# Kernel tuning notes

Hardware: AMD Instinct MI355X
Metric: run time of the kernel (lower is better)

## Reference

```python
import jax, jax.numpy as jnp
import numpy as np

N_NODES = 100000
N_EDGES = 1000000
D_FEAT = 64


def setup_inputs() -> dict:
    key = jax.random.key(0)
    k1, k2 = jax.random.split(key)
    x = jax.random.normal(k1, (N_NODES, D_FEAT), dtype=jnp.float32)
    es = jax.random.randint(k2, (2, N_EDGES), 0, N_NODES, dtype=jnp.int32)
    return {"x": x, "es": es}


def reference(x, es):
    # message (option='o2i'): col, row = es ; x_i = x[row], x_o = x[col]
    col, row = es[0], es[1]
    x_i = x[row]                              # [E, D]
    x_o = x[col]                              # [E, D]
    msg = jnp.concatenate([x_i, x_o], axis=-1)  # [E, 2D]
    n = x.shape[0]
    # aggregate: scatter-mean over idx=col
    summed = jax.ops.segment_sum(msg, col, num_segments=n)          # [N, 2D]
    ones = jnp.ones((es.shape[1],), dtype=x.dtype)
    count = jax.ops.segment_sum(ones, col, num_segments=n)          # [N]
    count = jnp.maximum(count, 1.0)[:, None]  # clamp(min=1), broadcast
    return summed / count
```

## Files before the change

### kernel.cpp

```cpp
#include <hip/hip_runtime.h>

#define D 64
#define SH 8
#define CPB 256
#define CH 2048
#define MAXNB 512


__global__ __launch_bounds__(256) void count_kernel(
    const int* __restrict__ es, int* __restrict__ cmat,
    int NB, int NBLK, int E) {
  __shared__ int hist[MAXNB];
  int t = threadIdx.x;
  hist[t] = 0;
  hist[t + 256] = 0;
  __syncthreads();
  int base_e = blockIdx.x * CH;
#pragma unroll
  for (int j = 0; j < 8; j++) {
    int e = base_e + t + j * 256;
    if (e < E) atomicAdd(&hist[es[e] >> SH], 1);
  }
  __syncthreads();
  for (int b = t; b < NB; b += 256) cmat[b * NBLK + blockIdx.x] = hist[b];
}

__global__ __launch_bounds__(256) void scanP1(
    int* __restrict__ cmat, int* __restrict__ bsums, int M) {
  __shared__ int lds[256];
  int t = threadIdx.x;
  int base = blockIdx.x * 1024 + t * 4;
  int v[4], s = 0;
#pragma unroll
  for (int i = 0; i < 4; i++) {
    v[i] = (base + i < M) ? cmat[base + i] : 0;
    s += v[i];
  }
  lds[t] = s;
  __syncthreads();
  for (int off = 1; off < 256; off <<= 1) {
    int val = (t >= off) ? lds[t - off] : 0;
    __syncthreads();
    lds[t] += val;
    __syncthreads();
  }
  int run = lds[t] - s;
#pragma unroll
  for (int i = 0; i < 4; i++) {
    if (base + i < M) cmat[base + i] = run;
    run += v[i];
  }
  if (t == 255) bsums[blockIdx.x] = lds[255];
}

__global__ __launch_bounds__(256) void scanP2(
    int* __restrict__ bsums, int* __restrict__ bbase,
    int* __restrict__ offsets, int nb, int NB, int N, int E) {
  __shared__ int lds[256];
  int t = threadIdx.x;
  int v = (t < nb) ? bsums[t] : 0;
  lds[t] = v;
  __syncthreads();
  for (int off = 1; off < 256; off <<= 1) {
    int val = (t >= off) ? lds[t - off] : 0;
    __syncthreads();
    lds[t] += val;
    __syncthreads();
  }
  if (t < nb) bsums[t] = lds[t] - v;
  if (t == 0) { bbase[NB] = E; offsets[N] = E; }
}

__global__ __launch_bounds__(256) void scanP3(
    int* __restrict__ cmat, const int* __restrict__ bsums,
    int* __restrict__ bbase, int M, int NBLK) {
  int t = threadIdx.x;
  int add = bsums[blockIdx.x];
  int base = blockIdx.x * 1024 + t * 4;
#pragma unroll
  for (int i = 0; i < 4; i++) {
    int idx = base + i;
    if (idx < M) {
      int v = cmat[idx] + add;
      cmat[idx] = v;
      if (idx % NBLK == 0) bbase[idx / NBLK] = v;
    }
  }
}

__global__ __launch_bounds__(256) void scatter_kernel(
    const int* __restrict__ es, const int* __restrict__ cmat,
    int* __restrict__ packed, int NB, int NBLK, int E) {
  __shared__ int hist[MAXNB];
  __shared__ int lstart[MAXNB];
  __shared__ int gbase[MAXNB];
  __shared__ int cursor[MAXNB];
  __shared__ int sctmp[256];
  __shared__ int staged[CH];
  __shared__ int bidl[CH];
  int t = threadIdx.x;
  hist[t] = 0;
  hist[t + 256] = 0;
  __syncthreads();
  int base_e = blockIdx.x * CH;
  int c[8], r[8];
#pragma unroll
  for (int j = 0; j < 8; j++) {
    int e = base_e + t + j * 256;
    if (e < E) {
      c[j] = es[e];
      r[j] = es[E + e];
      atomicAdd(&hist[c[j] >> SH], 1);
    } else {
      c[j] = -1;
    }
  }
  __syncthreads();
  int c0 = hist[2 * t], c1 = hist[2 * t + 1];
  int pair = c0 + c1;
  sctmp[t] = pair;
  __syncthreads();
  for (int off = 1; off < 256; off <<= 1) {
    int val = (t >= off) ? sctmp[t - off] : 0;
    __syncthreads();
    sctmp[t] += val;
    __syncthreads();
  }
  int excl = sctmp[t] - pair;
  lstart[2 * t] = excl;
  lstart[2 * t + 1] = excl + c0;
  cursor[2 * t] = excl;
  cursor[2 * t + 1] = excl + c0;
  for (int b = t; b < NB; b += 256) gbase[b] = cmat[b * NBLK + blockIdx.x];
  __syncthreads();
#pragma unroll
  for (int j = 0; j < 8; j++) {
    if (c[j] >= 0) {
      int b = c[j] >> SH;
      int rank = atomicAdd(&cursor[b], 1);
      staged[rank] = (r[j] << SH) | (c[j] & (CPB - 1));
      bidl[rank] = b;
    }
  }
  __syncthreads();
  int nloc = min(CH, E - base_e);
  for (int i = t; i < nloc; i += 256) {
    int b = bidl[i];
    packed[gbase[b] + (i - lstart[b])] = staged[i];
  }
}

__global__ __launch_bounds__(256) void sort_cols(
    const int* __restrict__ packed, const int* __restrict__ bbase,
    int* __restrict__ offsets, int* __restrict__ sorted_rows, int N) {
  __shared__ int cnt[CPB];
  __shared__ int sctmp[256];
  __shared__ int cur[CPB];
  int b = blockIdx.x;
  int t = threadIdx.x;
  int s = bbase[b], e = bbase[b + 1];
  cnt[t] = 0;
  __syncthreads();
  for (int i = s + t; i < e; i += 256) atomicAdd(&cnt[packed[i] & (CPB - 1)], 1);
  __syncthreads();
  int v = cnt[t];
  sctmp[t] = v;
  __syncthreads();
  for (int off = 1; off < 256; off <<= 1) {
    int val = (t >= off) ? sctmp[t - off] : 0;
    __syncthreads();
    sctmp[t] += val;
    __syncthreads();
  }
  int excl = sctmp[t] - v;
  cur[t] = excl;
  int gc = (b << SH) + t;
  if (gc < N) offsets[gc] = s + excl;
  __syncthreads();
  for (int i = s + t; i < e; i += 256) {
    int p = packed[i];
    int rank = atomicAdd(&cur[p & (CPB - 1)], 1);
    sorted_rows[s + rank] = p >> SH;
  }
}

__global__ __launch_bounds__(256) void node_reduce(
    const float4* __restrict__ x4, const int* __restrict__ sorted_rows,
    const int* __restrict__ offsets, float* __restrict__ out, int N) {
  int gid = blockIdx.x * 256 + threadIdx.x;
  int node = gid >> 6;
  if (node >= N) return;
  int lane = threadIdx.x & 63;
  int eg = lane >> 4;
  int d16 = lane & 15;
  int start = offsets[node];
  int cnt = offsets[node + 1] - start;
  float4 a0 = make_float4(0.f, 0.f, 0.f, 0.f);
  float4 a1 = make_float4(0.f, 0.f, 0.f, 0.f);
  float4 a2 = make_float4(0.f, 0.f, 0.f, 0.f);
  float4 a3 = make_float4(0.f, 0.f, 0.f, 0.f);
  for (int base = 0; base < cnt; base += 16) {
    int k0 = base + eg;
    int k1 = base + 4 + eg;
    int k2 = base + 8 + eg;
    int k3 = base + 12 + eg;
    int r0 = (k0 < cnt) ? sorted_rows[start + k0] : -1;
    int r1 = (k1 < cnt) ? sorted_rows[start + k1] : -1;
    int r2 = (k2 < cnt) ? sorted_rows[start + k2] : -1;
    int r3 = (k3 < cnt) ? sorted_rows[start + k3] : -1;
    if (r0 >= 0) { float4 v = x4[(size_t)r0 * 16 + d16];
      a0.x += v.x; a0.y += v.y; a0.z += v.z; a0.w += v.w; }
    if (r1 >= 0) { float4 v = x4[(size_t)r1 * 16 + d16];
      a1.x += v.x; a1.y += v.y; a1.z += v.z; a1.w += v.w; }
    if (r2 >= 0) { float4 v = x4[(size_t)r2 * 16 + d16];
      a2.x += v.x; a2.y += v.y; a2.z += v.z; a2.w += v.w; }
    if (r3 >= 0) { float4 v = x4[(size_t)r3 * 16 + d16];
      a3.x += v.x; a3.y += v.y; a3.z += v.z; a3.w += v.w; }
  }
  a0.x += a1.x + a2.x + a3.x;
  a0.y += a1.y + a2.y + a3.y;
  a0.z += a1.z + a2.z + a3.z;
  a0.w += a1.w + a2.w + a3.w;
  a0.x += __shfl_xor(a0.x, 16); a0.y += __shfl_xor(a0.y, 16);
  a0.z += __shfl_xor(a0.z, 16); a0.w += __shfl_xor(a0.w, 16);
  a0.x += __shfl_xor(a0.x, 32); a0.y += __shfl_xor(a0.y, 32);
  a0.z += __shfl_xor(a0.z, 32); a0.w += __shfl_xor(a0.w, 32);
  float4* o4 = (float4*)(out + (size_t)node * 2 * D);
  if (eg == 0) {
    float inv = 1.0f / (float)(cnt > 0 ? cnt : 1);
    a0.x *= inv; a0.y *= inv; a0.z *= inv; a0.w *= inv;
    o4[d16] = a0;
  } else if (eg == 1) {
    float4 v = (cnt > 0) ? x4[(size_t)node * 16 + d16]
                         : make_float4(0.f, 0.f, 0.f, 0.f);
    o4[16 + d16] = v;
  }
}


__global__ __launch_bounds__(256) void edge_scatter_atomic(
    const int* __restrict__ es, const float* __restrict__ x,
    float* __restrict__ out, int* __restrict__ count, int E) {
  int gid = blockIdx.x * blockDim.x + threadIdx.x;
  int e = gid >> 6;
  int lane = gid & 63;
  if (e >= E) return;
  int c = es[e];
  int r = es[E + e];
  if (lane == 0) atomicAdd(&count[c], 1);
  float v = x[(size_t)r * D + lane];
  unsafeAtomicAdd(&out[(size_t)c * 2 * D + lane], v);
}

__global__ __launch_bounds__(256) void finalize_atomic(
    const float* __restrict__ x, float* __restrict__ out,
    const int* __restrict__ count, int N) {
  int gid = blockIdx.x * blockDim.x + threadIdx.x;
  int node = gid >> 5;
  int j4 = gid & 31;
  if (node >= N) return;
  int cnt = count[node];
  float4* out4 = (float4*)(out + (size_t)node * 2 * D);
  if (j4 < 16) {
    float4 s = out4[j4];
    float inv = 1.0f / (float)(cnt > 0 ? cnt : 1);
    s.x *= inv; s.y *= inv; s.z *= inv; s.w *= inv;
    out4[j4] = s;
  } else {
    float4 v;
    if (cnt > 0) {
      const float4* x4 = (const float4*)(x + (size_t)node * D);
      v = x4[j4 - 16];
    } else {
      v = make_float4(0.f, 0.f, 0.f, 0.f);
    }
    out4[j4] = v;
  }
}

extern "C" void kernel_launch(void* const* d_in, const int* in_sizes, int n_in,
                              void* d_out, int out_size, void* d_ws, size_t ws_size,
                              hipStream_t stream) {
  const float* x = (const float*)d_in[0];
  const int* es = (const int*)d_in[1];
  int N = in_sizes[0] / D;
  int E = in_sizes[1] / 2;
  float* out = (float*)d_out;

  int NB = (N + CPB - 1) >> SH;
  int NBLK = (E + CH - 1) / CH;
  int M = NB * NBLK;
  int nb2 = (M + 1023) / 1024;
  size_t need = ((size_t)M + 256 + (NB + 1) + ((size_t)N + 1) +
                 2 * (size_t)E) * sizeof(int);
  if (NB > MAXNB || nb2 > 256 || ws_size < need) {
    int* count = (int*)d_ws;
    hipMemsetAsync(count, 0, (size_t)N * sizeof(int), stream);
    hipMemsetAsync(out, 0, (size_t)N * 2 * D * sizeof(float), stream);
    long long t1 = (long long)E * 64;
    edge_scatter_atomic<<<(int)((t1 + 255) / 256), 256, 0, stream>>>(es, x, out, count, E);
    long long t2 = (long long)N * 32;
    finalize_atomic<<<(int)((t2 + 255) / 256), 256, 0, stream>>>(x, out, count, N);
    return;
  }

  int* ws = (int*)d_ws;
  int* cmat = ws;
  int* bsums = cmat + M;
  int* bbase = bsums + 256;
  int* offsets = bbase + NB + 1;
  int* packed = offsets + N + 1;
  int* sorted_rows = packed + E;

  count_kernel<<<NBLK, 256, 0, stream>>>(es, cmat, NB, NBLK, E);
  scanP1<<<nb2, 256, 0, stream>>>(cmat, bsums, M);
  scanP2<<<1, 256, 0, stream>>>(bsums, bbase, offsets, nb2, NB, N, E);
  scanP3<<<nb2, 256, 0, stream>>>(cmat, bsums, bbase, M, NBLK);
  scatter_kernel<<<NBLK, 256, 0, stream>>>(es, cmat, packed, NB, NBLK, E);
  sort_cols<<<NB, 256, 0, stream>>>(packed, bbase, offsets, sorted_rows, N);

  long long rt = (long long)N * 64;
  node_reduce<<<(int)((rt + 255) / 256), 256, 0, stream>>>(
      (const float4*)x, sorted_rows, offsets, out, N);
}
```

Before: 156.9 us.

## Fuse counting-sort pipeline into one cooperative kernel with grid syncs

Replaces the six-kernel bucket-sort pipeline (count, three-pass scan, scatter, per-bucket sort) with a single cooperative kernel of 512 blocks that uses grid.sync between phases. Edges are kept in registers between the count and scatter phases, so the second read of the edge list goes away, and several launch boundaries are removed. In exchange, every phase is limited to a fixed grid of 512 blocks, all blocks must be co-resident, and each grid-wide barrier adds its own cost.

```diff
diff --git a/kernel.cpp b/kernel.cpp
--- a/kernel.cpp
+++ b/kernel.cpp
@@ -1,108 +1,37 @@
 #include <hip/hip_runtime.h>
+#include <hip/hip_cooperative_groups.h>
+
+namespace cg = cooperative_groups;
 
 #define D 64
 #define SH 8
 #define CPB 256
-#define CH 2048
-#define MAXNB 512
-
-
-__global__ __launch_bounds__(256) void count_kernel(
+#define MBLK 512
+#define MCH 2048
+
+__global__ __launch_bounds__(256) void mega(
     const int* __restrict__ es, int* __restrict__ cmat,
-    int NB, int NBLK, int E) {
-  __shared__ int hist[MAXNB];
+    int* __restrict__ bsums, int* __restrict__ packed,
+    int* __restrict__ offsets, int* __restrict__ sorted_rows,
+    int N, int E, int NB) {
+  cg::grid_group grid = cg::this_grid();
+  __shared__ int hist[512];
+  __shared__ int lstart[512];
+  __shared__ int gbase[512];
+  __shared__ int cursor[512];
+  __shared__ int sctmp[256];
+  __shared__ int staged[MCH];
+  __shared__ int bidl[MCH];
+  __shared__ int scnt[256];
+  __shared__ int scur[256];
   int t = threadIdx.x;
+  int blk = blockIdx.x;
+  const int NBLK = MBLK;
+
   hist[t] = 0;
   hist[t + 256] = 0;
   __syncthreads();
-  int base_e = blockIdx.x * CH;
-#pragma unroll
-  for (int j = 0; j < 8; j++) {
-    int e = base_e + t + j * 256;
-    if (e < E) atomicAdd(&hist[es[e] >> SH], 1);
-  }
-  __syncthreads();
-  for (int b = t; b < NB; b += 256) cmat[b * NBLK + blockIdx.x] = hist[b];
-}
-
-__global__ __launch_bounds__(256) void scanP1(
-    int* __restrict__ cmat, int* __restrict__ bsums, int M) {
-  __shared__ int lds[256];
-  int t = threadIdx.x;
-  int base = blockIdx.x * 1024 + t * 4;
-  int v[4], s = 0;
-#pragma unroll
-  for (int i = 0; i < 4; i++) {
-    v[i] = (base + i < M) ? cmat[base + i] : 0;
-    s += v[i];
-  }
-  lds[t] = s;
-  __syncthreads();
-  for (int off = 1; off < 256; off <<= 1) {
-    int val = (t >= off) ? lds[t - off] : 0;
-    __syncthreads();
-    lds[t] += val;
-    __syncthreads();
-  }
-  int run = lds[t] - s;
-#pragma unroll
-  for (int i = 0; i < 4; i++) {
-    if (base + i < M) cmat[base + i] = run;
-    run += v[i];
-  }
-  if (t == 255) bsums[blockIdx.x] = lds[255];
-}
-
-__global__ __launch_bounds__(256) void scanP2(
-    int* __restrict__ bsums, int* __restrict__ bbase,
-    int* __restrict__ offsets, int nb, int NB, int N, int E) {
-  __shared__ int lds[256];
-  int t = threadIdx.x;
-  int v = (t < nb) ? bsums[t] : 0;
-  lds[t] = v;
-  __syncthreads();
-  for (int off = 1; off < 256; off <<= 1) {
-    int val = (t >= off) ? lds[t - off] : 0;
-    __syncthreads();
-    lds[t] += val;
-    __syncthreads();
-  }
-  if (t < nb) bsums[t] = lds[t] - v;
-  if (t == 0) { bbase[NB] = E; offsets[N] = E; }
-}
-
-__global__ __launch_bounds__(256) void scanP3(
-    int* __restrict__ cmat, const int* __restrict__ bsums,
-    int* __restrict__ bbase, int M, int NBLK) {
-  int t = threadIdx.x;
-  int add = bsums[blockIdx.x];
-  int base = blockIdx.x * 1024 + t * 4;
-#pragma unroll
-  for (int i = 0; i < 4; i++) {
-    int idx = base + i;
-    if (idx < M) {
-      int v = cmat[idx] + add;
-      cmat[idx] = v;
-      if (idx % NBLK == 0) bbase[idx / NBLK] = v;
-    }
-  }
-}
-
-__global__ __launch_bounds__(256) void scatter_kernel(
-    const int* __restrict__ es, const int* __restrict__ cmat,
-    int* __restrict__ packed, int NB, int NBLK, int E) {
-  __shared__ int hist[MAXNB];
-  __shared__ int lstart[MAXNB];
-  __shared__ int gbase[MAXNB];
-  __shared__ int cursor[MAXNB];
-  __shared__ int sctmp[256];
-  __shared__ int staged[CH];
-  __shared__ int bidl[CH];
-  int t = threadIdx.x;
-  hist[t] = 0;
-  hist[t + 256] = 0;
-  __syncthreads();
-  int base_e = blockIdx.x * CH;
+  int base_e = blk * MCH;
   int c[8], r[8];
 #pragma unroll
   for (int j = 0; j < 8; j++) {
@@ -116,22 +45,72 @@
     }
   }
   __syncthreads();
-  int c0 = hist[2 * t], c1 = hist[2 * t + 1];
-  int pair = c0 + c1;
+  int h0 = hist[2 * t], h1 = hist[2 * t + 1];
+  int pair = h0 + h1;
   sctmp[t] = pair;
   __syncthreads();
   for (int off = 1; off < 256; off <<= 1) {
-    int val = (t >= off) ? sctmp[t - off] : 0;
-    __syncthreads();
-    sctmp[t] += val;
+    int v = (t >= off) ? sctmp[t - off] : 0;
+    __syncthreads();
+    sctmp[t] += v;
     __syncthreads();
   }
   int excl = sctmp[t] - pair;
   lstart[2 * t] = excl;
-  lstart[2 * t + 1] = excl + c0;
-  cursor[2 * t] = excl;
-  cursor[2 * t + 1] = excl + c0;
-  for (int b = t; b < NB; b += 256) gbase[b] = cmat[b * NBLK + blockIdx.x];
+  lstart[2 * t + 1] = excl + h0;
+  for (int b = t; b < NB; b += 256) cmat[b * NBLK + blk] = hist[b];
+  if (blk == 0 && t == 0) offsets[N] = E;
+  grid.sync();
+
+  int M = NB * NBLK;
+  int nch = (M + 1023) >> 10;
+  if (blk < nch) {
+    int base = blk * 1024 + t * 4;
+    int v0 = (base + 0 < M) ? cmat[base + 0] : 0;
+    int v1 = (base + 1 < M) ? cmat[base + 1] : 0;
+    int v2 = (base + 2 < M) ? cmat[base + 2] : 0;
+    int v3 = (base + 3 < M) ? cmat[base + 3] : 0;
+    int s = v0 + v1 + v2 + v3;
+    sctmp[t] = s;
+    __syncthreads();
+    for (int off = 1; off < 256; off <<= 1) {
+      int v = (t >= off) ? sctmp[t - off] : 0;
+      __syncthreads();
+      sctmp[t] += v;
+      __syncthreads();
+    }
+    int run = sctmp[t] - s;
+    if (base + 0 < M) cmat[base + 0] = run;
+    run += v0;
+    if (base + 1 < M) cmat[base + 1] = run;
+    run += v1;
+    if (base + 2 < M) cmat[base + 2] = run;
+    run += v2;
+    if (base + 3 < M) cmat[base + 3] = run;
+    if (t == 255) bsums[blk] = sctmp[255];
+  }
+  grid.sync();
+
+  if (blk == 0) {
+    int v = (t < nch) ? bsums[t] : 0;
+    sctmp[t] = v;
+    __syncthreads();
+    for (int off = 1; off < 256; off <<= 1) {
+      int u = (t >= off) ? sctmp[t - off] : 0;
+      __syncthreads();
+      sctmp[t] += u;
+      __syncthreads();
+    }
+    if (t < nch) bsums[t] = sctmp[t] - v;
+  }
+  grid.sync();
+
+  for (int b = t; b < NB; b += 256) {
+    int idx = b * NBLK + blk;
+    gbase[b] = cmat[idx] + bsums[idx >> 10];
+  }
+  cursor[t] = lstart[t];
+  cursor[t + 256] = lstart[t + 256];
   __syncthreads();
 #pragma unroll
   for (int j = 0; j < 8; j++) {
@@ -143,44 +122,47 @@
     }
   }
   __syncthreads();
-  int nloc = min(CH, E - base_e);
+  int nloc = min(MCH, E - base_e);
   for (int i = t; i < nloc; i += 256) {
     int b = bidl[i];
     packed[gbase[b] + (i - lstart[b])] = staged[i];
   }
-}
-
-__global__ __launch_bounds__(256) void sort_cols(
-    const int* __restrict__ packed, const int* __restrict__ bbase,
-    int* __restrict__ offsets, int* __restrict__ sorted_rows, int N) {
-  __shared__ int cnt[CPB];
-  __shared__ int sctmp[256];
-  __shared__ int cur[CPB];
-  int b = blockIdx.x;
-  int t = threadIdx.x;
-  int s = bbase[b], e = bbase[b + 1];
-  cnt[t] = 0;
-  __syncthreads();
-  for (int i = s + t; i < e; i += 256) atomicAdd(&cnt[packed[i] & (CPB - 1)], 1);
-  __syncthreads();
-  int v = cnt[t];
-  sctmp[t] = v;
-  __syncthreads();
-  for (int off = 1; off < 256; off <<= 1) {
-    int val = (t >= off) ? sctmp[t - off] : 0;
-    __syncthreads();
-    sctmp[t] += val;
-    __syncthreads();
-  }
-  int excl = sctmp[t] - v;
-  cur[t] = excl;
-  int gc = (b << SH) + t;
-  if (gc < N) offsets[gc] = s + excl;
-  __syncthreads();
-  for (int i = s + t; i < e; i += 256) {
-    int p = packed[i];
-    int rank = atomicAdd(&cur[p & (CPB - 1)], 1);
-    sorted_rows[s + rank] = p >> SH;
+  grid.sync();
+
+  if (blk < NB) {
+    int b = blk;
+    int i0 = b * NBLK;
+    int s = cmat[i0] + bsums[i0 >> 10];
+    int e;
+    if (b + 1 < NB) {
+      int i1 = (b + 1) * NBLK;
+      e = cmat[i1] + bsums[i1 >> 10];
+    } else {
+      e = E;
+    }
+    scnt[t] = 0;
+    __syncthreads();
+    for (int i = s + t; i < e; i += 256) atomicAdd(&scnt[packed[i] & (CPB - 1)], 1);
+    __syncthreads();
+    int v = scnt[t];
+    sctmp[t] = v;
+    __syncthreads();
+    for (int off = 1; off < 256; off <<= 1) {
+      int u = (t >= off) ? sctmp[t - off] : 0;
+      __syncthreads();
+      sctmp[t] += u;
+      __syncthreads();
+    }
+    int ex = sctmp[t] - v;
+    scur[t] = ex;
+    int gc = (b << SH) + t;
+    if (gc < N) offsets[gc] = s + ex;
+    __syncthreads();
+    for (int i = s + t; i < e; i += 256) {
+      int p = packed[i];
+      int rank = atomicAdd(&scur[p & (CPB - 1)], 1);
+      sorted_rows[s + rank] = p >> SH;
+    }
   }
 }
 
@@ -288,12 +270,10 @@
   float* out = (float*)d_out;
 
   int NB = (N + CPB - 1) >> SH;
-  int NBLK = (E + CH - 1) / CH;
-  int M = NB * NBLK;
-  int nb2 = (M + 1023) / 1024;
-  size_t need = ((size_t)M + 256 + (NB + 1) + ((size_t)N + 1) +
-                 2 * (size_t)E) * sizeof(int);
-  if (NB > MAXNB || nb2 > 256 || ws_size < need) {
+  int M = NB * MBLK;
+  size_t need = ((size_t)M + 256 + (size_t)N + 1 + 2 * (size_t)E) * sizeof(int);
+  bool fast = (NB <= 512) && (E <= MBLK * MCH) && (ws_size >= need);
+  if (!fast) {
     int* count = (int*)d_ws;
     hipMemsetAsync(count, 0, (size_t)N * sizeof(int), stream);
     hipMemsetAsync(out, 0, (size_t)N * 2 * D * sizeof(float), stream);
@@ -307,17 +287,14 @@
   int* ws = (int*)d_ws;
   int* cmat = ws;
   int* bsums = cmat + M;
-  int* bbase = bsums + 256;
-  int* offsets = bbase + NB + 1;
+  int* offsets = bsums + 256;
   int* packed = offsets + N + 1;
   int* sorted_rows = packed + E;
 
-  count_kernel<<<NBLK, 256, 0, stream>>>(es, cmat, NB, NBLK, E);
-  scanP1<<<nb2, 256, 0, stream>>>(cmat, bsums, M);
-  scanP2<<<1, 256, 0, stream>>>(bsums, bbase, offsets, nb2, NB, N, E);
-  scanP3<<<nb2, 256, 0, stream>>>(cmat, bsums, bbase, M, NBLK);
-  scatter_kernel<<<NBLK, 256, 0, stream>>>(es, cmat, packed, NB, NBLK, E);
-  sort_cols<<<NB, 256, 0, stream>>>(packed, bbase, offsets, sorted_rows, N);
+  void* args[] = {(void*)&es, (void*)&cmat, (void*)&bsums, (void*)&packed,
+                  (void*)&offsets, (void*)&sorted_rows,
+                  (void*)&N, (void*)&E, (void*)&NB};
+  hipLaunchCooperativeKernel((const void*)mega, dim3(MBLK), dim3(256), args, 0, stream);
 
   long long rt = (long long)N * 64;
   node_reduce<<<(int)((rt + 255) / 256), 256, 0, stream>>>(
```

Result: slower. 385.2 us (+145.4%).

## Fuse count and scan via last-block reduction, reserve bucket slots with global atomics

Applied to the files above, without the earlier changes.

Replaces the per-block count matrix and its three-pass scan with global per-bucket totals, where the last finishing block scans them. The scatter kernel now reserves each block's output range by atomically adding to per-bucket cursors instead of reading a precomputed prefix matrix. The edge chunk per block doubles and the bucket-id staging array is narrowed to 16-bit. This removes three kernel launches and the count-matrix traffic, at the cost of adding a memset and global atomic contention. Edge order within a bucket becomes nondeterministic, which changes floating-point summation order.

```diff
diff --git a/kernel.cpp b/kernel.cpp
--- a/kernel.cpp
+++ b/kernel.cpp
@@ -3,109 +3,79 @@
 #define D 64
 #define SH 8
 #define CPB 256
-#define CH 2048
+#define CH 4096
 #define MAXNB 512
 
-
-__global__ __launch_bounds__(256) void count_kernel(
-    const int* __restrict__ es, int* __restrict__ cmat,
-    int NB, int NBLK, int E) {
+__global__ __launch_bounds__(256) void count_scan(
+    const int* __restrict__ es, int* __restrict__ btot,
+    int* __restrict__ done, int* __restrict__ bbase,
+    int* __restrict__ cursor, int* __restrict__ offsets,
+    int NB, int E, int N) {
   __shared__ int hist[MAXNB];
+  __shared__ int sctmp[256];
+  __shared__ int lastflag;
   int t = threadIdx.x;
   hist[t] = 0;
   hist[t + 256] = 0;
   __syncthreads();
   int base_e = blockIdx.x * CH;
 #pragma unroll
-  for (int j = 0; j < 8; j++) {
+  for (int j = 0; j < 16; j++) {
     int e = base_e + t + j * 256;
     if (e < E) atomicAdd(&hist[es[e] >> SH], 1);
   }
   __syncthreads();
-  for (int b = t; b < NB; b += 256) cmat[b * NBLK + blockIdx.x] = hist[b];
-}
-
-__global__ __launch_bounds__(256) void scanP1(
-    int* __restrict__ cmat, int* __restrict__ bsums, int M) {
-  __shared__ int lds[256];
-  int t = threadIdx.x;
-  int base = blockIdx.x * 1024 + t * 4;
-  int v[4], s = 0;
-#pragma unroll
-  for (int i = 0; i < 4; i++) {
-    v[i] = (base + i < M) ? cmat[base + i] : 0;
-    s += v[i];
-  }
-  lds[t] = s;
+  for (int b = t; b < NB; b += 256) {
+    int h = hist[b];
+    if (h) atomicAdd(&btot[b], h);
+  }
+  __syncthreads();
+  if (t == 0) {
+    __threadfence();
+    int d = atomicAdd(done, 1);
+    lastflag = (d == (int)gridDim.x - 1);
+  }
+  __syncthreads();
+  if (!lastflag) return;
+  __threadfence();
+  int i0 = 2 * t, i1 = 2 * t + 1;
+  int h0 = (i0 < NB) ? __hip_atomic_load(&btot[i0], __ATOMIC_RELAXED,
+                                         __HIP_MEMORY_SCOPE_AGENT) : 0;
+  int h1 = (i1 < NB) ? __hip_atomic_load(&btot[i1], __ATOMIC_RELAXED,
+                                         __HIP_MEMORY_SCOPE_AGENT) : 0;
+  int pair = h0 + h1;
+  sctmp[t] = pair;
   __syncthreads();
   for (int off = 1; off < 256; off <<= 1) {
-    int val = (t >= off) ? lds[t - off] : 0;
-    __syncthreads();
-    lds[t] += val;
-    __syncthreads();
-  }
-  int run = lds[t] - s;
-#pragma unroll
-  for (int i = 0; i < 4; i++) {
-    if (base + i < M) cmat[base + i] = run;
-    run += v[i];
-  }
-  if (t == 255) bsums[blockIdx.x] = lds[255];
-}
-
-__global__ __launch_bounds__(256) void scanP2(
-    int* __restrict__ bsums, int* __restrict__ bbase,
-    int* __restrict__ offsets, int nb, int NB, int N, int E) {
-  __shared__ int lds[256];
-  int t = threadIdx.x;
-  int v = (t < nb) ? bsums[t] : 0;
-  lds[t] = v;
-  __syncthreads();
-  for (int off = 1; off < 256; off <<= 1) {
-    int val = (t >= off) ? lds[t - off] : 0;
-    __syncthreads();
-    lds[t] += val;
-    __syncthreads();
-  }
-  if (t < nb) bsums[t] = lds[t] - v;
+    int v = (t >= off) ? sctmp[t - off] : 0;
+    __syncthreads();
+    sctmp[t] += v;
+    __syncthreads();
+  }
+  int excl = sctmp[t] - pair;
+  if (i0 < NB) { bbase[i0] = excl; cursor[i0] = excl; }
+  if (i1 < NB) { bbase[i1] = excl + h0; cursor[i1] = excl + h0; }
   if (t == 0) { bbase[NB] = E; offsets[N] = E; }
 }
 
-__global__ __launch_bounds__(256) void scanP3(
-    int* __restrict__ cmat, const int* __restrict__ bsums,
-    int* __restrict__ bbase, int M, int NBLK) {
-  int t = threadIdx.x;
-  int add = bsums[blockIdx.x];
-  int base = blockIdx.x * 1024 + t * 4;
-#pragma unroll
-  for (int i = 0; i < 4; i++) {
-    int idx = base + i;
-    if (idx < M) {
-      int v = cmat[idx] + add;
-      cmat[idx] = v;
-      if (idx % NBLK == 0) bbase[idx / NBLK] = v;
-    }
-  }
-}
-
-__global__ __launch_bounds__(256) void scatter_kernel(
-    const int* __restrict__ es, const int* __restrict__ cmat,
-    int* __restrict__ packed, int NB, int NBLK, int E) {
+__global__ __launch_bounds__(256) void scatter_res(
+    const int* __restrict__ es, int* __restrict__ cursor,
+    int* __restrict__ packed, int NB, int E) {
   __shared__ int hist[MAXNB];
   __shared__ int lstart[MAXNB];
   __shared__ int gbase[MAXNB];
-  __shared__ int cursor[MAXNB];
+  __shared__ int lcur[MAXNB];
   __shared__ int sctmp[256];
   __shared__ int staged[CH];
-  __shared__ int bidl[CH];
+  __shared__ unsigned short bidl[CH];
   int t = threadIdx.x;
   hist[t] = 0;
   hist[t + 256] = 0;
   __syncthreads();
   int base_e = blockIdx.x * CH;
-  int c[8], r[8];
+  int c[16], r[16];
 #pragma unroll
-  for (int j = 0; j < 8; j++) {
+  for (int j = 0; j < 16; j++) {
     int e = base_e + t + j * 256;
     if (e < E) {
       c[j] = es[e];
@@ -116,30 +86,33 @@
     }
   }
   __syncthreads();
-  int c0 = hist[2 * t], c1 = hist[2 * t + 1];
-  int pair = c0 + c1;
+  int h0 = hist[2 * t], h1 = hist[2 * t + 1];
+  int pair = h0 + h1;
   sctmp[t] = pair;
   __syncthreads();
   for (int off = 1; off < 256; off <<= 1) {
-    int val = (t >= off) ? sctmp[t - off] : 0;
-    __syncthreads();
-    sctmp[t] += val;
+    int v = (t >= off) ? sctmp[t - off] : 0;
+    __syncthreads();
+    sctmp[t] += v;
     __syncthreads();
   }
   int excl = sctmp[t] - pair;
   lstart[2 * t] = excl;
-  lstart[2 * t + 1] = excl + c0;
-  cursor[2 * t] = excl;
-  cursor[2 * t + 1] = excl + c0;
-  for (int b = t; b < NB; b += 256) gbase[b] = cmat[b * NBLK + blockIdx.x];
+  lstart[2 * t + 1] = excl + h0;
+  lcur[2 * t] = excl;
+  lcur[2 * t + 1] = excl + h0;
+  for (int b = t; b < NB; b += 256) {
+    int h = hist[b];
+    gbase[b] = h ? atomicAdd(&cursor[b], h) : 0;
+  }
   __syncthreads();
 #pragma unroll
-  for (int j = 0; j < 8; j++) {
+  for (int j = 0; j < 16; j++) {
     if (c[j] >= 0) {
       int b = c[j] >> SH;
-      int rank = atomicAdd(&cursor[b], 1);
+      int rank = atomicAdd(&lcur[b], 1);
       staged[rank] = (r[j] << SH) | (c[j] & (CPB - 1));
-      bidl[rank] = b;
+      bidl[rank] = (unsigned short)b;
     }
   }
   __syncthreads();
@@ -167,9 +140,9 @@
   sctmp[t] = v;
   __syncthreads();
   for (int off = 1; off < 256; off <<= 1) {
-    int val = (t >= off) ? sctmp[t - off] : 0;
-    __syncthreads();
-    sctmp[t] += val;
+    int u = (t >= off) ? sctmp[t - off] : 0;
+    __syncthreads();
+    sctmp[t] += u;
     __syncthreads();
   }
   int excl = sctmp[t] - v;
@@ -289,11 +262,9 @@
 
   int NB = (N + CPB - 1) >> SH;
   int NBLK = (E + CH - 1) / CH;
-  int M = NB * NBLK;
-  int nb2 = (M + 1023) / 1024;
-  size_t need = ((size_t)M + 256 + (NB + 1) + ((size_t)N + 1) +
+  size_t need = ((size_t)NB + 1 + (NB + 1) + NB + ((size_t)N + 1) +
                  2 * (size_t)E) * sizeof(int);
-  if (NB > MAXNB || nb2 > 256 || ws_size < need) {
+  if (NB > MAXNB || ws_size < need) {
     int* count = (int*)d_ws;
     hipMemsetAsync(count, 0, (size_t)N * sizeof(int), stream);
     hipMemsetAsync(out, 0, (size_t)N * 2 * D * sizeof(float), stream);
@@ -305,18 +276,19 @@
   }
 
   int* ws = (int*)d_ws;
-  int* cmat = ws;
-  int* bsums = cmat + M;
-  int* bbase = bsums + 256;
-  int* offsets = bbase + NB + 1;
+  int* btot = ws;
+  int* done = btot + NB;
+  int* bbase = done + 1;
+  int* cursor = bbase + NB + 1;
+  int* offsets = cursor + NB;
   int* packed = offsets + N + 1;
   int* sorted_rows = packed + E;
 
-  count_kernel<<<NBLK, 256, 0, stream>>>(es, cmat, NB, NBLK, E);
-  scanP1<<<nb2, 256, 0, stream>>>(cmat, bsums, M);
-  scanP2<<<1, 256, 0, stream>>>(bsums, bbase, offsets, nb2, NB, N, E);
-  scanP3<<<nb2, 256, 0, stream>>>(cmat, bsums, bbase, M, NBLK);
-  scatter_kernel<<<NBLK, 256, 0, stream>>>(es, cmat, packed, NB, NBLK, E);
+  hipMemsetAsync(btot, 0, ((size_t)NB + 1) * sizeof(int), stream);
+
+  count_scan<<<NBLK, 256, 0, stream>>>(es, btot, done, bbase, cursor, offsets,
+                                       NB, E, N);
+  scatter_res<<<NBLK, 256, 0, stream>>>(es, cursor, packed, NB, E);
   sort_cols<<<NB, 256, 0, stream>>>(packed, bbase, offsets, sorted_rows, N);
 
   long long rt = (long long)N * 64;
```

After: 163.4 us. 4.1% more time.
